# Kernel tuning notes

Hardware: AMD Instinct MI355X
Metric: run time of the kernel (lower is better)

## Reference

```python
import jax, jax.numpy as jnp
from jax import lax
import numpy as np

DIM = 128
HEADS = 2
WS = 4            # window_size = int(44 / 11)
HIDDEN = 4 * DIM  # ffn_expansion_factor = 4


def setup_inputs() -> dict:
    key = jax.random.key(0)
    ks = jax.random.split(key, 16)
    b, c, h, w = 4, DIM, 88, 88
    s = 0.02
    return {
        "x": jax.random.normal(ks[0], (b, c, h, w), jnp.float32),
        "mask": jax.random.uniform(ks[1], (b, 1, 44, 44), jnp.float32),
        "edge_f": jax.random.normal(ks[2], (b, c, 44, 44), jnp.float32),
        "ln1_w": jnp.ones((c,), jnp.float32),
        "ln1_b": jnp.zeros((c,), jnp.float32),
        "Wq": jax.random.normal(ks[3], (c, c), jnp.float32) * s,
        "Wk": jax.random.normal(ks[4], (c, c), jnp.float32) * s,
        "Wv": jax.random.normal(ks[5], (c, c), jnp.float32) * s,
        "ln2_w": jnp.ones((c,), jnp.float32),
        "ln2_b": jnp.zeros((c,), jnp.float32),
        "w_in": jax.random.normal(ks[6], (2 * HIDDEN, c), jnp.float32) * s,      # 1x1 conv dim -> 2*hidden
        "w_dw": jax.random.normal(ks[7], (2 * HIDDEN, 1, 3, 3), jnp.float32) * s,  # depthwise 3x3
        "w_out": jax.random.normal(ks[8], (c, HIDDEN), jnp.float32) * s,          # 1x1 conv hidden -> dim
    }


def _layernorm_c(t, g, beta):
    # WithBias LayerNorm over the channel axis (to_3d normalizes last dim == c)
    mu = t.mean(axis=1, keepdims=True)
    var = t.var(axis=1, keepdims=True)
    return (t - mu) / jnp.sqrt(var + 1e-5) * g[None, :, None, None] + beta[None, :, None, None]


def _windows(t, ws):
    # (b,c,h,w) -> (b*h*w/ws^2, ws^2, c), matching torch view/permute/contiguous
    b, c, h, w = t.shape
    t = t.reshape(b, c, h // ws, ws, w // ws, ws)
    t = t.transpose(0, 2, 4, 3, 5, 1)  # b, h/ws, w/ws, ws, ws, c
    return t.reshape(-1, ws * ws, c)


def reference(x, mask, edge_f, ln1_w, ln1_b, Wq, Wk, Wv, ln2_w, ln2_b, w_in, w_dw, w_out):
    b, c, h, w = x.shape
    ws, heads = WS, HEADS
    dh = c // heads
    scale = dh ** (-0.5)

    # ---- Attention branch (norm1 -> windowed edge/mask-conditioned attention) ----
    xn = _layernorm_c(x, ln1_w, ln1_b)
    edge = jax.image.resize(edge_f, (b, c, h, w), method="bilinear")
    m = jax.image.resize(mask, (b, mask.shape[1], h, w), method="bilinear")

    q = _windows(edge, ws) @ Wq.T            # (Bw, ws^2, c); dropout inactive (eval)
    x0 = _windows(xn * m, ws)                # mask-modulated keys/values
    k = x0 @ Wk.T
    v = x0 @ Wv.T

    Bw = q.shape[0]
    q = q.reshape(Bw, ws * ws, heads, dh)
    k = k.reshape(Bw, ws * ws, heads, dh)
    v = v.reshape(Bw, ws * ws, heads, dh)

    # dots: per-token head_dim x head_dim matrix, summed over heads (as in the source einsum)
    dots = jnp.einsum("bnhj,bnhk->bnjk", q, k) * scale   # (Bw, ws^2, dh, dh)
    attn = jax.nn.softmax(dots, axis=-1)
    out = jnp.einsum("bnjk,bnhk->bnhj", attn, v)          # (Bw, ws^2, heads, dh)

    out = out.reshape(Bw, ws * ws, c)
    out = out.reshape(b, h // ws, w // ws, ws * ws * c)
    out = out.transpose(0, 3, 1, 2).reshape(b, c, h, w)   # scrambled view, faithful to source

    x = x + out

    # ---- FeedForward branch (norm2 -> gated dwconv FFN) ----
    xn2 = _layernorm_c(x, ln2_w, ln2_b)
    t = jnp.einsum("oc,bchw->bohw", w_in, xn2)            # 1x1 conv, no bias
    t = lax.conv_general_dilated(
        t, w_dw, (1, 1), "SAME",
        feature_group_count=w_dw.shape[0],
        dimension_numbers=("NCHW", "OIHW", "NCHW"))
    t1, t2 = jnp.split(t, 2, axis=1)
    t = jax.nn.gelu(t1, approximate=False) * t2
    out2 = jnp.einsum("oc,bchw->bohw", w_out, t)
    return x + out2
```

## Files before the change

kernel.cpp:

```cpp
#include <hip/hip_runtime.h>
#include <hip/hip_bf16.h>
#include <hip/hip_fp16.h>
#include <math.h>

#define BATCH 4
#define C 128
#define H 88
#define W 88
#define HW 7744
#define NPIX 30976
#define HALF 44
#define HID 512

#if defined(__has_builtin)
#  if __has_builtin(__builtin_amdgcn_exp2f)
#    define EXP_FAST(x) __builtin_amdgcn_exp2f(x)
#    define QSCALE 0.18033688011112042f
#  endif
#endif
#ifndef EXP_FAST
#  define EXP_FAST(x) __expf(x)
#  define QSCALE 0.125f
#endif

typedef __attribute__((ext_vector_type(8))) short bfrag;
typedef __attribute__((ext_vector_type(4))) float f32x4;

__device__ __forceinline__ short f2bf(float f) {
    union { __hip_bfloat16 b; unsigned short u; } cv;
    cv.b = __float2bfloat16(f);
    return (short)cv.u;
}
__device__ __forceinline__ float bf2f(short s) {
    union { unsigned int u; float f; } cv;
    cv.u = ((unsigned int)(unsigned short)s) << 16;
    return cv.f;
}
__device__ __forceinline__ bfrag cvt8(const float* p) {
    const float4 f0 = *(const float4*)p;
    const float4 f1 = *(const float4*)(p + 4);
    bfrag t;
    t[0] = f2bf(f0.x); t[1] = f2bf(f0.y); t[2] = f2bf(f0.z); t[3] = f2bf(f0.w);
    t[4] = f2bf(f1.x); t[5] = f2bf(f1.y); t[6] = f2bf(f1.z); t[7] = f2bf(f1.w);
    return t;
}

__device__ __forceinline__ unsigned char f2e5(float f) {
    union { __half h; unsigned short u; } cv;
    cv.h = __float2half(f);
    unsigned short lo = cv.u & 0xFF;
    unsigned short hi = cv.u >> 8;
    hi += (lo > 0x80 || (lo == 0x80 && (hi & 1))) ? 1 : 0;
    return (unsigned char)hi;
}
__device__ __forceinline__ float e52f(unsigned char b) {
    union { unsigned short u; __half h; } cv;
    cv.u = ((unsigned short)b) << 8;
    return __half2float(cv.h);
}

__device__ __forceinline__ void up_taps(int i, int& j0, int& j1, float& w0, float& w1) {
    float f = 0.5f * i - 0.25f;
    int i0 = (int)floorf(f);
    float fr = f - (float)i0;
    j0 = max(i0, 0);
    j1 = min(i0 + 1, HALF - 1);
    w0 = 1.f - fr;
    w1 = fr;
}

__global__ __launch_bounds__(256) void k_pre(
    const float* __restrict__ x, const float* __restrict__ mask,
    const float* __restrict__ edge, const float* __restrict__ ln1w,
    const float* __restrict__ ln1b,
    __hip_bfloat16* __restrict__ xnm, __hip_bfloat16* __restrict__ eo)
{
    __shared__ float redS[8][32], redQ[8][32];
    const int tid = threadIdx.x, s = tid >> 5, px = tid & 31;
    const int blk = blockIdx.x, b = blk / 242, hw0 = (blk % 242) * 32;
    const int hw = hw0 + px, hi = hw / W, wi = hw % W;
    const int cs = s * 16;

    int y0, y1, x0, x1c; float wy0, wy1, wx0, wx1;
    up_taps(hi, y0, y1, wy0, wy1);
    up_taps(wi, x0, x1c, wx0, wx1);

    const float* mb = mask + (size_t)b * HALF * HALF;
    const float mval = wy0 * (wx0 * mb[y0 * HALF + x0] + wx1 * mb[y0 * HALF + x1c])
                     + wy1 * (wx0 * mb[y1 * HALF + x0] + wx1 * mb[y1 * HALF + x1c]);

    const float* xb = x + (size_t)b * C * HW;
    const float* ebs = edge + (size_t)b * C * HALF * HALF;
    float xr[16], er[16];
    float sum = 0.f, sq = 0.f;
    #pragma unroll
    for (int i = 0; i < 16; ++i) {
        const int c = cs + i;
        const float t = xb[c * HW + hw];
        xr[i] = t; sum += t; sq += t * t;
        const float* ec = ebs + c * HALF * HALF;
        er[i] = wy0 * (wx0 * ec[y0 * HALF + x0] + wx1 * ec[y0 * HALF + x1c])
              + wy1 * (wx0 * ec[y1 * HALF + x0] + wx1 * ec[y1 * HALF + x1c]);
    }
    redS[s][px] = sum; redQ[s][px] = sq;
    __syncthreads();
    float tsum = 0.f, tsq = 0.f;
    #pragma unroll
    for (int i = 0; i < 8; ++i) { tsum += redS[i][px]; tsq += redQ[i][px]; }
    const float mu = tsum * (1.f / C);
    const float rstd = rsqrtf(tsq * (1.f / C) - mu * mu + 1e-5f);

    const size_t gp = (size_t)b * HW + hw;
    bfrag r0, r1;
    #pragma unroll
    for (int i = 0; i < 8; ++i) {
        r0[i] = f2bf(((xr[i] - mu) * rstd * ln1w[cs + i] + ln1b[cs + i]) * mval);
        r1[i] = f2bf(((xr[8 + i] - mu) * rstd * ln1w[cs + 8 + i] + ln1b[cs + 8 + i]) * mval);
    }
    *(bfrag*)((short*)xnm + gp * C + cs) = r0;
    *(bfrag*)((short*)xnm + gp * C + cs + 8) = r1;
    #pragma unroll
    for (int i = 0; i < 8; ++i) { r0[i] = f2bf(er[i]); r1[i] = f2bf(er[8 + i]); }
    *(bfrag*)((short*)eo + gp * C + cs) = r0;
    *(bfrag*)((short*)eo + gp * C + cs + 8) = r1;
}


__global__ __launch_bounds__(512) void k_gemmQKV(
    const __hip_bfloat16* __restrict__ eb, const __hip_bfloat16* __restrict__ xnm,
    const float* __restrict__ Wq, const float* __restrict__ Wk, const float* __restrict__ Wv,
    __hip_bfloat16* __restrict__ qb, __hip_bfloat16* __restrict__ kb,
    __hip_bfloat16* __restrict__ vb)
{
    __shared__ short Bs[64 * 136];
    const int mat = blockIdx.y >> 1;
    const int c0 = (blockIdx.y & 1) * 64;
    const __hip_bfloat16* A; const float* Wf; __hip_bfloat16* Out;
    if (mat == 0)      { A = eb;  Wf = Wq; Out = qb; }
    else if (mat == 1) { A = xnm; Wf = Wk; Out = kb; }
    else               { A = xnm; Wf = Wv; Out = vb; }

    const int tid = threadIdx.x;
    {
        const int sr = tid & 63, sq = tid >> 6;
        const float* wr = Wf + (size_t)(c0 + sr) * 128 + sq * 16;
        short* dstS = &Bs[sr * 136 + sq * 16];
        *(bfrag*)dstS = cvt8(wr);
        *(bfrag*)(dstS + 8) = cvt8(wr + 8);
    }
    __syncthreads();

    const int lane = tid & 63, wv = tid >> 6;
    const int wm = wv & 3, wn = wv >> 2;
    const int px0 = blockIdx.x * 128 + wm * 32;
    const int lcb = wn * 32;
    const int lr = lane & 15, lg = lane >> 4;
    const short* As = (const short*)A;

    f32x4 acc[2][2];
    #pragma unroll
    for (int i = 0; i < 2; ++i)
        #pragma unroll
        for (int j = 0; j < 2; ++j)
            #pragma unroll
            for (int r = 0; r < 4; ++r) acc[i][j][r] = 0.f;

    bfrag a_[4][2], b_[2][2];
    #pragma unroll
    for (int ks = 0; ks < 4; ++ks)
        #pragma unroll
        for (int mi = 0; mi < 2; ++mi)
            a_[ks][mi] = *(const bfrag*)(As + (size_t)(px0 + mi * 16 + lr) * 128 + ks * 32 + lg * 8);
    #pragma unroll
    for (int nj = 0; nj < 2; ++nj)
        b_[0][nj] = *(const bfrag*)&Bs[(lcb + nj * 16 + lr) * 136 + lg * 8];

    #pragma unroll
    for (int ks = 0; ks < 4; ++ks) {
        if (ks < 3) {
            #pragma unroll
            for (int nj = 0; nj < 2; ++nj)
                b_[(ks + 1) & 1][nj] = *(const bfrag*)&Bs[(lcb + nj * 16 + lr) * 136 + (ks + 1) * 32 + lg * 8];
        }
        #pragma unroll
        for (int mi = 0; mi < 2; ++mi)
            #pragma unroll
            for (int nj = 0; nj < 2; ++nj)
                acc[mi][nj] = __builtin_amdgcn_mfma_f32_16x16x32_bf16(a_[ks][mi], b_[ks & 1][nj], acc[mi][nj], 0, 0, 0);
    }
    short* Os = (short*)Out;
    #pragma unroll
    for (int mi = 0; mi < 2; ++mi)
        #pragma unroll
        for (int nj = 0; nj < 2; ++nj)
            #pragma unroll
            for (int r = 0; r < 4; ++r) {
                const int p = px0 + mi * 16 + lg * 4 + r;
                const int c = c0 + lcb + nj * 16 + lr;
                Os[(size_t)p * 128 + c] = f2bf(acc[mi][nj][r]);
            }
}

__global__ __launch_bounds__(512) void k_gemm128(
    const __hip_bfloat16* __restrict__ A,
    const float* __restrict__ Wf,
    unsigned char* __restrict__ Out)
{
    __shared__ short Bs[64 * 136];
    const int gc0 = blockIdx.y * 64;
    const int tid = threadIdx.x;
    {
        const int sr = tid & 63, sq = tid >> 6;
        const float* wr = Wf + (size_t)(gc0 + sr) * 128 + sq * 16;
        short* dstS = &Bs[sr * 136 + sq * 16];
        *(bfrag*)dstS = cvt8(wr);
        *(bfrag*)(dstS + 8) = cvt8(wr + 8);
    }
    __syncthreads();

    const int lane = tid & 63, wv = tid >> 6;
    const int wm = wv & 3, wn = wv >> 2;
    const int px0 = blockIdx.x * 128 + wm * 32;
    const int lcb = wn * 32;
    const int lr = lane & 15, lg = lane >> 4;
    const short* As = (const short*)A;

    f32x4 acc[2][2];
    #pragma unroll
    for (int i = 0; i < 2; ++i)
        #pragma unroll
        for (int j = 0; j < 2; ++j)
            #pragma unroll
            for (int r = 0; r < 4; ++r) acc[i][j][r] = 0.f;

    bfrag a_[4][2], b_[2][2];
    #pragma unroll
    for (int ks = 0; ks < 4; ++ks)
        #pragma unroll
        for (int mi = 0; mi < 2; ++mi)
            a_[ks][mi] = *(const bfrag*)(As + (size_t)(px0 + mi * 16 + lr) * 128 + ks * 32 + lg * 8);
    #pragma unroll
    for (int nj = 0; nj < 2; ++nj)
        b_[0][nj] = *(const bfrag*)&Bs[(lcb + nj * 16 + lr) * 136 + lg * 8];

    #pragma unroll
    for (int ks = 0; ks < 4; ++ks) {
        if (ks < 3) {
            #pragma unroll
            for (int nj = 0; nj < 2; ++nj)
                b_[(ks + 1) & 1][nj] = *(const bfrag*)&Bs[(lcb + nj * 16 + lr) * 136 + (ks + 1) * 32 + lg * 8];
        }
        #pragma unroll
        for (int mi = 0; mi < 2; ++mi)
            #pragma unroll
            for (int nj = 0; nj < 2; ++nj)
                acc[mi][nj] = __builtin_amdgcn_mfma_f32_16x16x32_bf16(a_[ks][mi], b_[ks & 1][nj], acc[mi][nj], 0, 0, 0);
    }
    #pragma unroll
    for (int mi = 0; mi < 2; ++mi)
        #pragma unroll
        for (int nj = 0; nj < 2; ++nj)
            #pragma unroll
            for (int r = 0; r < 4; ++r) {
                const int p = px0 + mi * 16 + lg * 4 + r;
                const int c = gc0 + lcb + nj * 16 + lr;
                Out[(size_t)p * 1024 + c] = f2e5(acc[mi][nj][r]);
            }
}

__global__ __launch_bounds__(512) void k_attn3(
    const __hip_bfloat16* __restrict__ Q, const __hip_bfloat16* __restrict__ Kb,
    const __hip_bfloat16* __restrict__ Vb, __hip_bfloat16* __restrict__ att)
{
    __shared__ float kv[64][32][4];
    const int tid = threadIdx.x, s = tid >> 5, px = tid & 31;
    const int blk = blockIdx.x, b = blk / 242, hw0 = (blk % 242) * 32;
    const size_t gp = (size_t)b * HW + hw0 + px;
    const int cs = s * 8;

    {
        const short* ks_ = (const short*)Kb + gp * C + cs;
        const short* vs_ = (const short*)Vb + gp * C + cs;
        bfrag kb0 = *(const bfrag*)ks_;
        bfrag vb0 = *(const bfrag*)vs_;
        const int comp = (s < 8) ? 0 : 1;
        const int kkb = (s & 7) * 8;
        #pragma unroll
        for (int i = 0; i < 8; ++i) {
            kv[kkb + i][px][comp]     = bf2f(kb0[i]);
            kv[kkb + i][px][comp + 2] = bf2f(vb0[i]);
        }
    }
    float q1r[4], q2r[4];
    {
        const short* qs = (const short*)Q + gp * C;
        #pragma unroll
        for (int rr = 0; rr < 4; ++rr) {
            const int j = s + 16 * rr;
            q1r[rr] = bf2f(qs[j]) * QSCALE;
            q2r[rr] = bf2f(qs[64 + j]) * QSCALE;
        }
    }
    __syncthreads();

    float ssum[4], o1[4], o2[4];
    #pragma unroll
    for (int rr = 0; rr < 4; ++rr) { ssum[rr] = 0.f; o1[rr] = 0.f; o2[rr] = 0.f; }

    #pragma unroll 8
    for (int kk = 0; kk < 64; ++kk) {
        const f32x4 vv = *(const f32x4*)kv[kk][px];
        #pragma unroll
        for (int rr = 0; rr < 4; ++rr) {
            const float d = q1r[rr] * vv[0] + q2r[rr] * vv[1];
            const float e = EXP_FAST(d);
            ssum[rr] += e;
            o1[rr] += e * vv[2];
            o2[rr] += e * vv[3];
        }
    }
    __syncthreads();
    float* vTT = &kv[0][0][0];
    #pragma unroll
    for (int rr = 0; rr < 4; ++rr) {
        const int j = s + 16 * rr;
        const float inv = 1.f / ssum[rr];
        vTT[px * 137 + j]      = o1[rr] * inv;
        vTT[px * 137 + 64 + j] = o2[rr] * inv;
    }
    __syncthreads();
    const int pxw = tid >> 4, c8 = (tid & 15) * 8;
    const size_t gpw = (size_t)b * HW + hw0 + pxw;
    bfrag r0;
    #pragma unroll
    for (int i = 0; i < 8; ++i) r0[i] = f2bf(vTT[pxw * 137 + c8 + i]);
    *(bfrag*)((short*)att + gpw * C + c8) = r0;
}

__global__ __launch_bounds__(256) void k_resid(
    const float* __restrict__ x, const __hip_bfloat16* __restrict__ att,
    const float* __restrict__ ln2w, const float* __restrict__ ln2b,
    __hip_bfloat16* __restrict__ x1, __hip_bfloat16* __restrict__ xn2)
{
    __shared__ float redS[8][32], redQ[8][32];
    const int tid = threadIdx.x, s = tid >> 5, px = tid & 31;
    const int blk = blockIdx.x, b = blk / 242, hw0 = (blk % 242) * 32;
    const int hw = hw0 + px;
    const int cs = s * 16;
    const int q = hw / 484, wbase = hw - q * 484;
    const int r_ = wbase / 22, col = wbase - r_ * 22;
    const short* attS = (const short*)att;
    const size_t bb = (size_t)b * HW;

    float v[16];
    float sum = 0.f, sq = 0.f;
    #pragma unroll
    for (int i = 0; i < 16; ++i) {
        const int c = cs + i;
        const int n = c >> 3;
        const int cj = 16 * (c & 7) + q;
        const int shi = r_ * 4 + (n >> 2), swi = col * 4 + (n & 3);
        const size_t gps = bb + (size_t)shi * W + swi;
        const float o = bf2f(attS[gps * C + cj]);
        const float xv = x[((size_t)b * C + c) * HW + hw];
        const float vv = xv + o;
        v[i] = vv; sum += vv; sq += vv * vv;
        x1[((size_t)b * C + c) * HW + hw] = __float2bfloat16(vv);
    }
    redS[s][px] = sum; redQ[s][px] = sq;
    __syncthreads();
    float tsum = 0.f, tsq = 0.f;
    #pragma unroll
    for (int i = 0; i < 8; ++i) { tsum += redS[i][px]; tsq += redQ[i][px]; }
    const float mu = tsum * (1.f / C);
    const float rstd = rsqrtf(tsq * (1.f / C) - mu * mu + 1e-5f);
    const size_t gp = bb + hw;
    bfrag r0, r1;
    #pragma unroll
    for (int i = 0; i < 8; ++i) {
        r0[i] = f2bf((v[i] - mu) * rstd * ln2w[cs + i] + ln2b[cs + i]);
        r1[i] = f2bf((v[8 + i] - mu) * rstd * ln2w[cs + 8 + i] + ln2b[cs + 8 + i]);
    }
    *(bfrag*)((short*)xn2 + gp * C + cs) = r0;
    *(bfrag*)((short*)xn2 + gp * C + cs + 8) = r1;
}

__global__ __launch_bounds__(512) void k_dw(
    const unsigned char* __restrict__ U,
    const float* __restrict__ wdw,
    __hip_bfloat16* __restrict__ Gout)
{
    const int cl = threadIdx.x;
    const int blk = blockIdx.x;
    const int seg = blk % 11;
    const int hi = (blk / 11) % H;
    const int b = blk / (11 * H);
    const int w0 = seg * 8;
    const int gc1 = cl, gc2 = 512 + cl;

    float w1[9], w2[9];
    #pragma unroll
    for (int t = 0; t < 9; ++t) { w1[t] = wdw[gc1 * 9 + t]; w2[t] = wdw[gc2 * 9 + t]; }

    const size_t base = (size_t)b * HW;
    const bool r0ok = (hi - 1) >= 0, r2ok = (hi + 1) < H;

    float A1[3][3], A2[3][3];

    #define LOADCOL(slot, wc)  do {                                              \
        if ((unsigned)(wc) >= W) {                                               \
            A1[slot][0]=A1[slot][1]=A1[slot][2]=0.f;                             \
            A2[slot][0]=A2[slot][1]=A2[slot][2]=0.f;                             \
        } else {                                                                 \
            size_t p1 = base + (size_t)(hi - 1) * W + (wc);                      \
            size_t p2 = base + (size_t)hi * W + (wc);                            \
            size_t p3 = base + (size_t)(hi + 1) * W + (wc);                      \
            A1[slot][0] = r0ok ? e52f(U[p1 * 1024 + cl]) : 0.f;                  \
            A2[slot][0] = r0ok ? e52f(U[p1 * 1024 + 512 + cl]) : 0.f;            \
            A1[slot][1] = e52f(U[p2 * 1024 + cl]);                               \
            A2[slot][1] = e52f(U[p2 * 1024 + 512 + cl]);                         \
            A1[slot][2] = r2ok ? e52f(U[p3 * 1024 + cl]) : 0.f;                  \
            A2[slot][2] = r2ok ? e52f(U[p3 * 1024 + 512 + cl]) : 0.f;            \
        } } while (0)

    LOADCOL(0, w0 - 1);
    LOADCOL(1, w0);

    #pragma unroll
    for (int i = 0; i < 8; ++i) {
        const int wi = w0 + i;
        const int sl = i % 3, sm = (i + 1) % 3, sr = (i + 2) % 3;
        LOADCOL(sr, wi + 1);
        float t1 = 0.f, t2 = 0.f;
        #pragma unroll
        for (int r = 0; r < 3; ++r) {
            t1 += w1[r * 3 + 0] * A1[sl][r] + w1[r * 3 + 1] * A1[sm][r] + w1[r * 3 + 2] * A1[sr][r];
            t2 += w2[r * 3 + 0] * A2[sl][r] + w2[r * 3 + 1] * A2[sm][r] + w2[r * 3 + 2] * A2[sr][r];
        }
        const float gl = 0.5f * t1 * (1.f + erff(t1 * 0.70710678118654752f));
        Gout[(base + (size_t)hi * W + wi) * 512 + cl] = __float2bfloat16(gl * t2);
    }
    #undef LOADCOL
}

__global__ __launch_bounds__(512) void k_gemm512(
    const __hip_bfloat16* __restrict__ G,
    const float* __restrict__ Wof,
    const __hip_bfloat16* __restrict__ X1,
    float* __restrict__ Outp)
{
    __shared__ short Bs[64 * 520];
    const int c0 = blockIdx.y * 64;
    const int tid = threadIdx.x;
    {
        const int sr = tid & 63, sq = tid >> 6;
        const float* wr = Wof + (size_t)(c0 + sr) * 512 + sq * 64;
        short* dstS = &Bs[sr * 520 + sq * 64];
        #pragma unroll
        for (int i8 = 0; i8 < 8; ++i8)
            *(bfrag*)(dstS + i8 * 8) = cvt8(wr + i8 * 8);
    }
    __syncthreads();

    const int lane = tid & 63, wv = tid >> 6;
    const int wm = wv & 3, wn = wv >> 2;
    const int px0 = blockIdx.x * 128 + wm * 32;
    const int lcb = wn * 32;
    const int lr = lane & 15, lg = lane >> 4;
    const short* Gs = (const short*)G;

    f32x4 acc[2][2];
    #pragma unroll
    for (int i = 0; i < 2; ++i)
        #pragma unroll
        for (int j = 0; j < 2; ++j)
            #pragma unroll
            for (int r = 0; r < 4; ++r) acc[i][j][r] = 0.f;

    bfrag a_[4][2], b_[2][2];
    #pragma unroll
    for (int ks = 0; ks < 4; ++ks)
        #pragma unroll
        for (int mi = 0; mi < 2; ++mi)
            a_[ks][mi] = *(const bfrag*)(Gs + (size_t)(px0 + mi * 16 + lr) * 512 + ks * 32 + lg * 8);
    #pragma unroll
    for (int nj = 0; nj < 2; ++nj)
        b_[0][nj] = *(const bfrag*)&Bs[(lcb + nj * 16 + lr) * 520 + lg * 8];

    #pragma unroll
    for (int ks = 0; ks < 16; ++ks) {
        if (ks < 15) {
            #pragma unroll
            for (int nj = 0; nj < 2; ++nj)
                b_[(ks + 1) & 1][nj] = *(const bfrag*)&Bs[(lcb + nj * 16 + lr) * 520 + (ks + 1) * 32 + lg * 8];
        }
        if (ks < 12) {
            #pragma unroll
            for (int mi = 0; mi < 2; ++mi)
                a_[(ks + 4) & 3][mi] = *(const bfrag*)(Gs + (size_t)(px0 + mi * 16 + lr) * 512 + (ks + 4) * 32 + lg * 8);
        }
        #pragma unroll
        for (int mi = 0; mi < 2; ++mi)
            #pragma unroll
            for (int nj = 0; nj < 2; ++nj)
                acc[mi][nj] = __builtin_amdgcn_mfma_f32_16x16x32_bf16(a_[ks & 3][mi], b_[ks & 1][nj], acc[mi][nj], 0, 0, 0);
    }

    #pragma unroll
    for (int mi = 0; mi < 2; ++mi)
        #pragma unroll
        for (int nj = 0; nj < 2; ++nj)
            #pragma unroll
            for (int r = 0; r < 4; ++r) {
                const int p = px0 + mi * 16 + lg * 4 + r;
                const int c = c0 + lcb + nj * 16 + lr;
                const int b = p / HW, hw = p % HW;
                const size_t idx = ((size_t)b * C + c) * HW + hw;
                Outp[idx] = __bfloat162float(X1[idx]) + acc[mi][nj][r];
            }
}

extern "C" void kernel_launch(void* const* d_in, const int* in_sizes, int n_in,
                              void* d_out, int out_size, void* d_ws, size_t ws_size,
                              hipStream_t stream) {
    (void)in_sizes; (void)n_in; (void)out_size; (void)ws_size;
    const float* x     = (const float*)d_in[0];
    const float* mask  = (const float*)d_in[1];
    const float* edge  = (const float*)d_in[2];
    const float* ln1w  = (const float*)d_in[3];
    const float* ln1b  = (const float*)d_in[4];
    const float* Wq    = (const float*)d_in[5];
    const float* Wk    = (const float*)d_in[6];
    const float* Wv    = (const float*)d_in[7];
    const float* ln2w  = (const float*)d_in[8];
    const float* ln2b  = (const float*)d_in[9];
    const float* w_in  = (const float*)d_in[10];
    const float* w_dw  = (const float*)d_in[11];
    const float* w_out = (const float*)d_in[12];
    float* out = (float*)d_out;

    char* ws = (char*)d_ws;
    __hip_bfloat16* x1  = (__hip_bfloat16*)(ws + 0);
    __hip_bfloat16* xn2 = (__hip_bfloat16*)(ws + 7929856);
    unsigned char*  u8  = (unsigned char*)(ws + 15859712);
    __hip_bfloat16* g   = (__hip_bfloat16*)(ws + 47579136);
    __hip_bfloat16* qb  = (__hip_bfloat16*)(ws + 15859712);
    __hip_bfloat16* kb  = (__hip_bfloat16*)(ws + 23789568);
    __hip_bfloat16* vb  = (__hip_bfloat16*)(ws + 31719424);
    __hip_bfloat16* eb  = (__hip_bfloat16*)(ws + 39649280);
    __hip_bfloat16* att = (__hip_bfloat16*)(ws + 39649280);
    __hip_bfloat16* xnm = (__hip_bfloat16*)(ws + 47579136);

    k_pre<<<968, 256, 0, stream>>>(x, mask, edge, ln1w, ln1b, xnm, eb);
    k_gemmQKV<<<dim3(242, 6), 512, 0, stream>>>(eb, xnm, Wq, Wk, Wv, qb, kb, vb);
    k_attn3<<<968, 512, 0, stream>>>(qb, kb, vb, att);
    k_resid<<<968, 256, 0, stream>>>(x, att, ln2w, ln2b, x1, xn2);
    k_gemm128<<<dim3(242, 16), 512, 0, stream>>>(xn2, w_in, u8);
    k_dw<<<3872, 512, 0, stream>>>(u8, w_dw, g);
    k_gemm512<<<dim3(242, 2), 512, 0, stream>>>(g, w_out, x1, out);
}
```

Measured before the change: 228.7 us.

## Store FFN-in activations channel-major in fp8 and vectorize depthwise conv loads

The 1x1 input GEMM now packs its e5m2 outputs through a shared-memory transpose and writes them channel-major (channel x pixel) with 16-byte stores, instead of scattered byte stores into a pixel-major layout. The depthwise 3x3 kernel then reads 16 consecutive pixels per row per channel with one uint4 load. It unpacks them with the hardware bf8-to-f32 conversion when that builtin exists, and accumulates all 8 outputs with compile-time-specialized tap code. This targets the uncoalesced byte-granular global traffic on both sides, at the cost of an extra LDS round trip and sync in the GEMM and some redundant halo loads.

```diff
diff --git a/kernel.cpp b/kernel.cpp
--- a/kernel.cpp
+++ b/kernel.cpp
@@ -17,6 +17,9 @@
 #    define EXP_FAST(x) __builtin_amdgcn_exp2f(x)
 #    define QSCALE 0.18033688011112042f
 #  endif
+#  if __has_builtin(__builtin_amdgcn_cvt_pk_f32_bf8)
+#    define HAS_BF8_CVT 1
+#  endif
 #endif
 #ifndef EXP_FAST
 #  define EXP_FAST(x) __expf(x)
@@ -57,6 +60,74 @@
     union { unsigned short u; __half h; } cv;
     cv.u = ((unsigned short)b) << 8;
     return __half2float(cv.h);
+}
+template<bool HI_>
+__device__ __forceinline__ void cvt2(unsigned int dw, float& a, float& b) {
+#ifdef HAS_BF8_CVT
+    auto r = __builtin_amdgcn_cvt_pk_f32_bf8((int)dw, HI_);
+    a = r[0]; b = r[1];
+#else
+    const unsigned short us = HI_ ? (unsigned short)(dw >> 16) : (unsigned short)(dw & 0xFFFFu);
+    a = e52f((unsigned char)(us & 0xFF));
+    b = e52f((unsigned char)(us >> 8));
+#endif
+}
+template<int D> __device__ __forceinline__ unsigned int dsel(const uint4& v) {
+    if constexpr (D == 0) return v.x;
+    else if constexpr (D == 1) return v.y;
+    else if constexpr (D == 2) return v.z;
+    else return v.w;
+}
+
+template<int K, int KLO, int KHI>
+__device__ __forceinline__ void acck(float x1a, float x1b, float x1c,
+                                     float x2a, float x2b, float x2c,
+                                     const float* w1, const float* w2,
+                                     float* acc1, float* acc2) {
+    if constexpr (K >= KLO && K <= KHI) {
+        if constexpr (K - 1 >= 0 && K - 1 <= 7) {
+            acc1[K-1] += x1a*w1[2] + x1b*w1[5] + x1c*w1[8];
+            acc2[K-1] += x2a*w2[2] + x2b*w2[5] + x2c*w2[8];
+        }
+        if constexpr (K >= 0 && K <= 7) {
+            acc1[K]   += x1a*w1[1] + x1b*w1[4] + x1c*w1[7];
+            acc2[K]   += x2a*w2[1] + x2b*w2[4] + x2c*w2[7];
+        }
+        if constexpr (K + 1 >= 0 && K + 1 <= 7) {
+            acc1[K+1] += x1a*w1[0] + x1b*w1[3] + x1c*w1[6];
+            acc2[K+1] += x2a*w2[0] + x2b*w2[3] + x2c*w2[6];
+        }
+    }
+}
+template<int BP, int SHIFT, int KLO, int KHI>
+__device__ __forceinline__ void dopair(const uint4* L1, const uint4* L2,
+                                       const float* w1, const float* w2,
+                                       float* acc1, float* acc2) {
+    constexpr int D = BP >> 1;
+    constexpr bool HI_ = (BP & 1) != 0;
+    float a1[3], b1[3], a2[3], b2[3];
+    #pragma unroll
+    for (int r = 0; r < 3; ++r) {
+        cvt2<HI_>(dsel<D>(L1[r]), a1[r], b1[r]);
+        cvt2<HI_>(dsel<D>(L2[r]), a2[r], b2[r]);
+    }
+    constexpr int K0 = 2 * BP - SHIFT;
+    acck<K0,     KLO, KHI>(a1[0], a1[1], a1[2], a2[0], a2[1], a2[2], w1, w2, acc1, acc2);
+    acck<K0 + 1, KLO, KHI>(b1[0], b1[1], b1[2], b2[0], b2[1], b2[2], w1, w2, acc1, acc2);
+}
+template<int SHIFT, int KLO, int KHI>
+__device__ __forceinline__ void dw_accum(const uint4* L1, const uint4* L2,
+                                         const float* w1, const float* w2,
+                                         float* acc1, float* acc2) {
+    constexpr int BPLO = (KLO + SHIFT) / 2;
+    constexpr int BPHI = (KHI + SHIFT) / 2;
+    if constexpr (BPLO <= 0 && 0 <= BPHI) dopair<0, SHIFT, KLO, KHI>(L1, L2, w1, w2, acc1, acc2);
+    if constexpr (BPLO <= 1 && 1 <= BPHI) dopair<1, SHIFT, KLO, KHI>(L1, L2, w1, w2, acc1, acc2);
+    if constexpr (BPLO <= 2 && 2 <= BPHI) dopair<2, SHIFT, KLO, KHI>(L1, L2, w1, w2, acc1, acc2);
+    if constexpr (BPLO <= 3 && 3 <= BPHI) dopair<3, SHIFT, KLO, KHI>(L1, L2, w1, w2, acc1, acc2);
+    if constexpr (BPLO <= 4 && 4 <= BPHI) dopair<4, SHIFT, KLO, KHI>(L1, L2, w1, w2, acc1, acc2);
+    if constexpr (BPLO <= 5 && 5 <= BPHI) dopair<5, SHIFT, KLO, KHI>(L1, L2, w1, w2, acc1, acc2);
+    if constexpr (BPLO <= 6 && 6 <= BPHI) dopair<6, SHIFT, KLO, KHI>(L1, L2, w1, w2, acc1, acc2);
 }
 
 __device__ __forceinline__ void up_taps(int i, int& j0, int& j1, float& w0, float& w1) {
@@ -207,6 +278,7 @@
     unsigned char* __restrict__ Out)
 {
     __shared__ short Bs[64 * 136];
+    __shared__ unsigned int T32[64][33];
     const int gc0 = blockIdx.y * 64;
     const int tid = threadIdx.x;
     {
@@ -259,13 +331,19 @@
     #pragma unroll
     for (int mi = 0; mi < 2; ++mi)
         #pragma unroll
-        for (int nj = 0; nj < 2; ++nj)
-            #pragma unroll
-            for (int r = 0; r < 4; ++r) {
-                const int p = px0 + mi * 16 + lg * 4 + r;
-                const int c = gc0 + lcb + nj * 16 + lr;
-                Out[(size_t)p * 1024 + c] = f2e5(acc[mi][nj][r]);
-            }
+        for (int nj = 0; nj < 2; ++nj) {
+            unsigned int pkv = 0;
+            #pragma unroll
+            for (int r = 0; r < 4; ++r)
+                pkv |= ((unsigned int)f2e5(acc[mi][nj][r])) << (8 * r);
+            T32[lcb + nj * 16 + lr][wm * 8 + mi * 4 + lg] = pkv;
+        }
+    __syncthreads();
+    const int cL = tid >> 3;
+    const int pw = (tid & 7) * 4;
+    uint4 vv;
+    vv.x = T32[cL][pw]; vv.y = T32[cL][pw + 1]; vv.z = T32[cL][pw + 2]; vv.w = T32[cL][pw + 3];
+    *(uint4*)(Out + (size_t)(gc0 + cL) * NPIX + (size_t)blockIdx.x * 128 + (size_t)pw * 4) = vv;
 }
 
 __global__ __launch_bounds__(512) void k_attn3(
@@ -390,57 +468,47 @@
     const float* __restrict__ wdw,
     __hip_bfloat16* __restrict__ Gout)
 {
-    const int cl = threadIdx.x;
+    const int c = threadIdx.x;
     const int blk = blockIdx.x;
     const int seg = blk % 11;
     const int hi = (blk / 11) % H;
     const int b = blk / (11 * H);
-    const int w0 = seg * 8;
-    const int gc1 = cl, gc2 = 512 + cl;
 
     float w1[9], w2[9];
     #pragma unroll
-    for (int t = 0; t < 9; ++t) { w1[t] = wdw[gc1 * 9 + t]; w2[t] = wdw[gc2 * 9 + t]; }
-
-    const size_t base = (size_t)b * HW;
-    const bool r0ok = (hi - 1) >= 0, r2ok = (hi + 1) < H;
-
-    float A1[3][3], A2[3][3];
-
-    #define LOADCOL(slot, wc)  do {                                              \
-        if ((unsigned)(wc) >= W) {                                               \
-            A1[slot][0]=A1[slot][1]=A1[slot][2]=0.f;                             \
-            A2[slot][0]=A2[slot][1]=A2[slot][2]=0.f;                             \
-        } else {                                                                 \
-            size_t p1 = base + (size_t)(hi - 1) * W + (wc);                      \
-            size_t p2 = base + (size_t)hi * W + (wc);                            \
-            size_t p3 = base + (size_t)(hi + 1) * W + (wc);                      \
-            A1[slot][0] = r0ok ? e52f(U[p1 * 1024 + cl]) : 0.f;                  \
-            A2[slot][0] = r0ok ? e52f(U[p1 * 1024 + 512 + cl]) : 0.f;            \
-            A1[slot][1] = e52f(U[p2 * 1024 + cl]);                               \
-            A2[slot][1] = e52f(U[p2 * 1024 + 512 + cl]);                         \
-            A1[slot][2] = r2ok ? e52f(U[p3 * 1024 + cl]) : 0.f;                  \
-            A2[slot][2] = r2ok ? e52f(U[p3 * 1024 + 512 + cl]) : 0.f;            \
-        } } while (0)
-
-    LOADCOL(0, w0 - 1);
-    LOADCOL(1, w0);
-
+    for (int t = 0; t < 9; ++t) { w1[t] = wdw[c * 9 + t]; w2[t] = wdw[(512 + c) * 9 + t]; }
+
+    const int start = (seg == 0) ? 0 : seg * 8 - 4;
+    uint4 L1[3], L2[3];
+    #pragma unroll
+    for (int r = 0; r < 3; ++r) {
+        const int row = hi + r - 1;
+        if ((unsigned)row < H) {
+            const size_t off = (size_t)b * HW + (size_t)row * W + start;
+            L1[r] = *(const uint4*)(U + (size_t)c * NPIX + off);
+            L2[r] = *(const uint4*)(U + (size_t)(512 + c) * NPIX + off);
+        } else {
+            L1[r] = make_uint4(0, 0, 0, 0);
+            L2[r] = make_uint4(0, 0, 0, 0);
+        }
+    }
+
+    float acc1[8], acc2[8];
+    #pragma unroll
+    for (int i = 0; i < 8; ++i) { acc1[i] = 0.f; acc2[i] = 0.f; }
+
+    if (seg == 0)       dw_accum<0,  0, 8>(L1, L2, w1, w2, acc1, acc2);
+    else if (seg == 10) dw_accum<4, -1, 7>(L1, L2, w1, w2, acc1, acc2);
+    else                dw_accum<4, -1, 8>(L1, L2, w1, w2, acc1, acc2);
+
+    short* Gs = (short*)Gout;
+    const size_t prow = (size_t)b * HW + (size_t)hi * W + seg * 8;
     #pragma unroll
     for (int i = 0; i < 8; ++i) {
-        const int wi = w0 + i;
-        const int sl = i % 3, sm = (i + 1) % 3, sr = (i + 2) % 3;
-        LOADCOL(sr, wi + 1);
-        float t1 = 0.f, t2 = 0.f;
-        #pragma unroll
-        for (int r = 0; r < 3; ++r) {
-            t1 += w1[r * 3 + 0] * A1[sl][r] + w1[r * 3 + 1] * A1[sm][r] + w1[r * 3 + 2] * A1[sr][r];
-            t2 += w2[r * 3 + 0] * A2[sl][r] + w2[r * 3 + 1] * A2[sm][r] + w2[r * 3 + 2] * A2[sr][r];
-        }
+        const float t1 = acc1[i], t2 = acc2[i];
         const float gl = 0.5f * t1 * (1.f + erff(t1 * 0.70710678118654752f));
-        Gout[(base + (size_t)hi * W + wi) * 512 + cl] = __float2bfloat16(gl * t2);
-    }
-    #undef LOADCOL
+        Gs[(prow + i) * 512 + c] = f2bf(gl * t2);
+    }
 }
 
 __global__ __launch_bounds__(512) void k_gemm512(
```

New measurement: 237.7 us. +4.0%, slower.
